# Optimization experiments

Hardware: AMD Instinct MI355X
Metric: run time of the kernel (lower is better)

The kernel has to match this reference:

```python
import jax, jax.numpy as jnp
import numpy as np

B, N, NFEAT = 8, 5000, 15
NUM_CLASSES_IN = 12          # len(elem_labels)
D_IN = NUM_CLASSES_IN + NFEAT - 1  # 26
D_DIST = 256
D_HID = 256
BIN_SIZE = 100
NBINS = N // BIN_SIZE        # 50
K = 16                       # num_neighbors
DIST_MULT = 0.1
MAX_HALF_BINS = 100          # max_num_bins // 2
NUM_ID_OUT, NUM_REG_OUT = 8, 4


def _pairwise_dist(A):
    # A: [nbins, bs, d] -> [nbins, bs, bs]
    na = jnp.sum(A * A, -1)
    d2 = na[..., :, None] - 2.0 * jnp.einsum('...nd,...md->...nm', A, A) + na[..., None, :]
    return jnp.sqrt(jnp.maximum(d2, 1e-6))


def _build_edges(points, rot):
    # points: [N, D_DIST]; LSH binning then per-bin kNN (exp(-dist_mult * dist) affinities)
    mul = points @ rot[:, :NBINS // 2]
    cmul = jnp.concatenate([mul, -mul], axis=-1)
    bin_idx = jnp.argmax(cmul, axis=-1)
    bins_split = jnp.argsort(bin_idx).reshape(NBINS, BIN_SIZE)   # [nbins, bs] point ids
    parts = points[bins_split]                                   # [nbins, bs, d]
    dm = jnp.exp(-DIST_MULT * _pairwise_dist(parts))             # [nbins, bs, bs]
    vals, idx = jax.lax.top_k(dm, K)                             # [nbins, bs, K]
    dst = jax.vmap(lambda b, i: b[i])(bins_split, idx)           # global dst ids
    src = jnp.broadcast_to(bins_split[:, :, None], dst.shape)
    return src.reshape(-1), dst.reshape(-1), vals.reshape(-1)    # nnz = N*K


def _ghconv(x, src, dst, vals, theta, W_h, W_t, b_t):
    # x: [N, H]; edge list (src, dst, vals); duplicates sum, matching tf.sparse.add
    deg = jax.ops.segment_sum(vals, src, num_segments=N)
    norm = jnp.power(deg + 1e-6, -0.5)[:, None]
    f_hom = (x @ theta) * norm
    agg = jax.ops.segment_sum(vals[:, None] * f_hom[dst], src, num_segments=N) * norm
    f_het = x @ W_h
    gate = jax.nn.sigmoid(x @ W_t + b_t)
    return jax.nn.selu(gate * agg + (1.0 - gate) * f_het)


def setup_inputs() -> dict:
    key = jax.random.key(0)
    ks = jax.random.split(key, 32)
    w = lambda i, shape, s=0.02: (s * jax.random.normal(ks[i], shape)).astype(jnp.float32)
    ids = jax.random.randint(ks[0], (B, N, 1), 0, NUM_CLASSES_IN).astype(jnp.float32)
    props = jax.random.normal(ks[1], (B, N, NFEAT - 1), dtype=jnp.float32)
    X = jnp.concatenate([ids, props], axis=-1)
    return {
        'X': X,
        'rot': w(2, (D_DIST, MAX_HALF_BINS), 1.0),
        'W_emb': w(3, (D_IN, D_DIST)), 'b_emb': w(4, (D_DIST,)),
        'Wenc_id': w(5, (D_IN, D_HID)), 'benc_id': w(6, (D_HID,)),
        'theta_id': w(7, (D_HID, D_HID)), 'Wh_id': w(8, (D_HID, D_HID)),
        'Wt_id': w(9, (D_HID, D_HID)), 'bt_id': w(10, (D_HID,)),
        'Wdec_id': w(11, (D_HID, D_HID)), 'bdec_id': w(12, (D_HID,)),
        'Wout_id': w(13, (D_HID, NUM_ID_OUT)), 'bout_id': w(14, (NUM_ID_OUT,)),
        'Wenc_reg': w(15, (D_IN, D_HID)), 'benc_reg': w(16, (D_HID,)),
        'theta_reg': w(17, (D_HID, D_HID)), 'Wh_reg': w(18, (D_HID, D_HID)),
        'Wt_reg': w(19, (D_HID, D_HID)), 'bt_reg': w(20, (D_HID,)),
        'Wdec_reg': w(21, (D_HID, D_HID)), 'bdec_reg': w(22, (D_HID,)),
        'Wout_reg': w(23, (D_HID, NUM_REG_OUT)), 'bout_reg': w(24, (NUM_REG_OUT,)),
    }


def reference(X, rot, W_emb, b_emb,
              Wenc_id, benc_id, theta_id, Wh_id, Wt_id, bt_id, Wdec_id, bdec_id, Wout_id, bout_id,
              Wenc_reg, benc_reg, theta_reg, Wh_reg, Wt_reg, bt_reg, Wdec_reg, bdec_reg, Wout_reg, bout_reg):
    # InputEncoding: one-hot class id + remaining features
    enc = jnp.concatenate(
        [jax.nn.one_hot(X[:, :, 0].astype(jnp.int32), NUM_CLASSES_IN, dtype=jnp.float32),
         X[:, :, 1:]], axis=-1)                                  # [B, N, 26]
    emb = enc @ W_emb + b_emb                                     # distance embedding
    src, dst, vals = jax.vmap(_build_edges, in_axes=(0, None))(emb, rot)

    def branch(Wenc, benc, theta, Wh, Wt, bt, Wdec, bdec, Wout, bout):
        x = jax.nn.selu(enc @ Wenc + benc)
        x = jax.vmap(lambda xb, s, d, v: _ghconv(xb, s, d, v, theta, Wh, Wt, bt))(x, src, dst, vals)
        x = jax.nn.selu(x @ Wdec + bdec)
        return x @ Wout + bout

    out_id = branch(Wenc_id, benc_id, theta_id, Wh_id, Wt_id, bt_id, Wdec_id, bdec_id, Wout_id, bout_id)
    out_reg = branch(Wenc_reg, benc_reg, theta_reg, Wh_reg, Wt_reg, bt_reg, Wdec_reg, bdec_reg, Wout_reg, bout_reg)
    return out_id, out_reg
```

## Files before the change

kernel.cpp:

```cpp
#include <hip/hip_runtime.h>
#include <hip/hip_bf16.h>
#include <cstdint>
#include <cstddef>

#define NB     8
#define NLOC   5000
#define NPTS   40000
#define DIN    26
#define DH     256
#define NBINS  50
#define BSZ    100
#define KNN    16
#define KP     104

static const size_t OFF_BHI0  = 40960000;
static const size_t OFF_BLO0  = 41353216;
static const size_t OFF_BDHI0 = 41746432;
static const size_t OFF_BDLO0 = 41877504;
static const size_t OFF_BHI1  = 42100000;
static const size_t OFF_BLO1  = 42493216;
static const size_t OFF_BDHI1 = 42886432;
static const size_t OFF_BDLO1 = 43017504;
static const size_t OFF_ENC   = 81920000;
static const size_t OFF_BIN   = 86080000;
static const size_t OFF_ORD   = 86240000;
static const size_t OFF_NRM   = 86400000;
static const size_t OFF_EVAL  = 86560000;
static const size_t OFF_EDST  = 89120000;
static const size_t OFF_KEYS  = 91680000;
static const size_t OFF_AXHI  = 91680000;
static const size_t OFF_AXLO  = 112160000;
static const size_t OFF_NA    = 132640000;
static const size_t OFF_FHET  = 132640000;
static const size_t OFF_GATE  = 173600000;

typedef __attribute__((ext_vector_type(8))) short short8;
typedef __attribute__((ext_vector_type(4))) float f32x4;

__device__ __forceinline__ float selu_f(float x) {
  const float scale = 1.0507009873554805f, alpha = 1.6732632423543772f;
  return x > 0.f ? scale * x : scale * alpha * expm1f(x);
}

__device__ __forceinline__ void split_bf16(float v, __hip_bfloat16& h, __hip_bfloat16& l) {
  h = __float2bfloat16(v);
  l = __float2bfloat16(v - __bfloat162float(h));
}

#define EPB 16
__global__ __launch_bounds__(256) void k_enc_emb(
    const float* __restrict__ X, const float* __restrict__ Wemb,
    const float* __restrict__ bemb, float* __restrict__ enc,
    double* __restrict__ emb, double* __restrict__ na_u) {
  __shared__ float xb[EPB * 15];
  __shared__ double partd[EPB][4];
  const int tid = threadIdx.x;
  const int lane = tid & 63, wid = tid >> 6;
  const int r0 = blockIdx.x * EPB;
  if (tid < EPB * 15) xb[tid] = X[(size_t)r0 * 15 + tid];
  double wcol[DIN];
  #pragma unroll
  for (int c = 0; c < DIN; c++) wcol[c] = (double)Wemb[c * DH + tid];
  const double bcol = (double)bemb[tid];
  __syncthreads();
  #pragma unroll 1
  for (int p = 0; p < EPB; p++) {
    const int id = (int)xb[p * 15];
    double acc = 0.0;
    #pragma unroll
    for (int c = 0; c < 12; c++)
      acc += ((c == id) ? 1.0 : 0.0) * wcol[c];
    #pragma unroll
    for (int c = 12; c < DIN; c++)
      acc += (double)xb[p * 15 + (c - 11)] * wcol[c];
    const double v = acc + bcol;
    emb[(size_t)(r0 + p) * DH + tid] = v;
    double sq = v * v;
    #pragma unroll
    for (int off = 32; off >= 1; off >>= 1) sq += __shfl_xor(sq, off);
    if (lane == 0) partd[p][wid] = sq;
  }
  __syncthreads();
  if (tid < EPB)
    na_u[r0 + tid] = partd[tid][0] + partd[tid][1] + partd[tid][2] + partd[tid][3];
  #pragma unroll
  for (int t = 0; t < 2; t++) {
    int idx = t * 256 + tid;
    if (idx < EPB * DIN) {
      int p = idx / DIN, c = idx - p * DIN;
      int id = (int)xb[p * 15];
      float v = (c < 12) ? ((c == id) ? 1.f : 0.f) : xb[p * 15 + (c - 11)];
      enc[(size_t)(r0 + p) * DIN + c] = v;
    }
  }
}

#define MULPTS 16
__global__ __launch_bounds__(512) void k_mul(
    const double* __restrict__ emb, const float* __restrict__ rot,
    int* __restrict__ bin_idx) {
  __shared__ double ebuf[MULPTS][258];
  __shared__ float  rotT[25][257];
  __shared__ double mulb[MULPTS][26];
  const int tid = threadIdx.x;
  const int r0 = blockIdx.x * MULPTS;
  for (int idx = tid; idx < 25 * DH; idx += 512) {
    int d = idx / 25, j = idx - d * 25;
    rotT[j][d] = rot[d * 100 + j];
  }
  for (int idx = tid; idx < MULPTS * DH; idx += 512) {
    int p = idx >> 8, d = idx & 255;
    ebuf[p][d] = emb[(size_t)(r0 + p) * DH + d];
  }
  __syncthreads();
  if (tid < MULPTS * 25) {
    int p = tid / 25, j = tid - p * 25;
    double a = 0.0;
    #pragma unroll 4
    for (int d = 0; d < DH; d++) a += ebuf[p][d] * (double)rotT[j][d];
    mulb[p][j] = a;
  }
  __syncthreads();
  if (tid < MULPTS) {
    double best = -1e300; int bi = 0;
    #pragma unroll 1
    for (int jj = 0; jj < 2 * 25; jj++) {
      double v = (jj < 25) ? mulb[tid][jj] : -mulb[tid][jj - 25];
      if (v > best) { best = v; bi = jj; }
    }
    bin_idx[r0 + tid] = bi;
  }
}

#define SCH 20
__global__ __launch_bounds__(256) void k_sort(
    const int* __restrict__ bin_idx, int* __restrict__ order) {
  const int b = blockIdx.x;
  __shared__ unsigned short cnt[256][NBINS + 2];
  __shared__ int base[NBINS];
  __shared__ int bl[NLOC];
  const int tid = threadIdx.x;
  for (int j = 0; j < NBINS; j++) cnt[tid][j] = 0;
  for (int n = tid; n < NLOC; n += 256) bl[n] = bin_idx[b * NLOC + n];
  __syncthreads();
  const int s = tid * SCH;
  const int e = (s + SCH < NLOC) ? s + SCH : NLOC;
  for (int n = s; n < e; n++) cnt[tid][bl[n]]++;
  __syncthreads();
  if (tid < NBINS) {
    int run = 0;
    for (int t = 0; t < 256; t++) {
      int c = cnt[t][tid];
      cnt[t][tid] = (unsigned short)run;
      run += c;
    }
    base[tid] = run;
  }
  __syncthreads();
  if (tid == 0) {
    int r = 0;
    for (int j = 0; j < NBINS; j++) { int t = base[j]; base[j] = r; r += t; }
  }
  __syncthreads();
  for (int n = s; n < e; n++) {
    int j = bl[n];
    int pos = base[j] + cnt[tid][j];
    cnt[tid][j]++;
    order[b * NLOC + pos] = n;
  }
}

#define DQR 112
__global__ __launch_bounds__(256) void k_dist(
    const double* __restrict__ emb, const int* __restrict__ order,
    const double* __restrict__ na_u, double* __restrict__ keys) {
  __shared__ double P[DQR][34];
  __shared__ double naL[DQR];
  __shared__ int rid[DQR];
  const int bin = blockIdx.x;
  const int gb0 = bin * BSZ;
  const int brow = (bin / NBINS) * NLOC;
  const int tid = threadIdx.x;
  const int tx = tid & 15, ty = tid >> 4;
  if (tid < DQR) {
    int rr = tid < BSZ ? tid : BSZ - 1;
    int g = brow + order[gb0 + rr];
    rid[tid] = g;
    naL[tid] = na_u[g];
  }
  __syncthreads();
  size_t srow[7];
  int scol[7], sr[7];
  #pragma unroll
  for (int q = 0; q < 7; q++) {
    int idx = q * 256 + tid;
    sr[q] = idx >> 4;
    scol[q] = (idx & 15) * 2;
    srow[q] = (size_t)rid[sr[q]] * DH;
  }
  double acc[7][7] = {};
  double2 buf[7];
  #pragma unroll
  for (int q = 0; q < 7; q++)
    buf[q] = *(const double2*)&emb[srow[q] + scol[q]];
  for (int kc = 0; kc < 8; kc++) {
    __syncthreads();
    #pragma unroll
    for (int q = 0; q < 7; q++) {
      P[sr[q]][scol[q]]     = buf[q].x;
      P[sr[q]][scol[q] + 1] = buf[q].y;
    }
    __syncthreads();
    if (kc < 7) {
      #pragma unroll
      for (int q = 0; q < 7; q++)
        buf[q] = *(const double2*)&emb[srow[q] + (kc + 1) * 32 + scol[q]];
    }
    #pragma unroll 1
    for (int kk = 0; kk < 32; kk += 2) {
      double2 b2[7], a2[7];
      #pragma unroll
      for (int j = 0; j < 7; j++) b2[j] = *(const double2*)&P[tx + 16 * j][kk];
      #pragma unroll
      for (int i = 0; i < 7; i++) a2[i] = *(const double2*)&P[ty + 16 * i][kk];
      #pragma unroll
      for (int i = 0; i < 7; i++)
        #pragma unroll
        for (int j = 0; j < 7; j++) acc[i][j] += a2[i].x * b2[j].x;
      #pragma unroll
      for (int i = 0; i < 7; i++)
        #pragma unroll
        for (int j = 0; j < 7; j++) acc[i][j] += a2[i].y * b2[j].y;
    }
  }
  #pragma unroll
  for (int i = 0; i < 7; i++) {
    int gi = ty + 16 * i;
    if (gi >= BSZ) continue;
    #pragma unroll
    for (int j = 0; j < 7; j++) {
      int gj = tx + 16 * j;
      if (gj >= BSZ) continue;
      double t = naL[gi] - 2.0 * acc[i][j];
      t += naL[gj];
      keys[(size_t)(gb0 + gi) * KP + gj] = (t > 1e-6) ? t : 1e-6;
    }
  }
}

__global__ __launch_bounds__(256) void k_topk(
    const double* __restrict__ keys, float* __restrict__ evals,
    int* __restrict__ edstl, float* __restrict__ normv) {
  const int g = threadIdx.x >> 4;
  const int l = threadIdx.x & 15;
  const int row = blockIdx.x * 16 + g;
  const unsigned long long* kr =
      (const unsigned long long*)(keys + (size_t)row * KP);
  unsigned long long c[7];
  #pragma unroll
  for (int s = 0; s < 7; s++) {
    int j = s * 16 + l;
    c[s] = (j < BSZ) ? kr[j] : ~0ull;
  }
  float deg = 0.f, myev = 0.f;
  int myidx = 0;
  #pragma unroll 1
  for (int k = 0; k < KNN; k++) {
    unsigned long long mv = c[0];
    int ms = 0;
    #pragma unroll
    for (int s = 1; s < 7; s++)
      if (c[s] < mv) { mv = c[s]; ms = s; }
    int idx = ms * 16 + l;
    #pragma unroll
    for (int off = 8; off >= 1; off >>= 1) {
      unsigned long long ov = __shfl_xor(mv, off);
      int oi = __shfl_xor(idx, off);
      if (ov < mv || (ov == mv && oi < idx)) { mv = ov; idx = oi; }
    }
    float ev = expf(-0.1f * sqrtf((float)__longlong_as_double(mv)));
    deg += ev;
    if (l == k) { myev = ev; myidx = idx; }
    const int own = idx & 15, slot = idx >> 4;
    if (l == own) {
      #pragma unroll
      for (int s = 0; s < 7; s++)
        if (slot == s) c[s] = ~0ull;
    }
  }
  evals[(size_t)row * KNN + l] = myev;
  edstl[(size_t)row * KNN + l] = myidx;
  if (l == 0) normv[row] = 1.f / sqrtf(deg + 1e-6f);
}

#define XPB 16
__global__ __launch_bounds__(256) void k_encmm(
    const float* __restrict__ enc, const float* __restrict__ W,
    const float* __restrict__ bias, __hip_bfloat16* __restrict__ hi,
    __hip_bfloat16* __restrict__ lo) {
  __shared__ float eb[XPB * DIN];
  const int tid = threadIdx.x;
  const int r0 = blockIdx.x * XPB;
  for (int idx = tid; idx < XPB * DIN; idx += 256)
    eb[idx] = enc[(size_t)r0 * DIN + idx];
  float wcol[DIN];
  #pragma unroll
  for (int c = 0; c < DIN; c++) wcol[c] = W[c * DH + tid];
  const float bcol = bias[tid];
  __syncthreads();
  #pragma unroll 1
  for (int p = 0; p < XPB; p++) {
    float acc = 0.f;
    #pragma unroll
    for (int c = 0; c < DIN; c++) acc += eb[p * DIN + c] * wcol[c];
    float v = selu_f(acc + bcol);
    __hip_bfloat16 h, l;
    split_bf16(v, h, l);
    hi[(size_t)(r0 + p) * DH + tid] = h;
    lo[(size_t)(r0 + p) * DH + tid] = l;
  }
}

__global__ __launch_bounds__(256) void k_cvt_w8(
    const float* __restrict__ W0, const float* __restrict__ W1,
    const float* __restrict__ W2, const float* __restrict__ W3,
    const float* __restrict__ W4, const float* __restrict__ W5,
    const float* __restrict__ W6, const float* __restrict__ W7,
    __hip_bfloat16* __restrict__ Bhi0, __hip_bfloat16* __restrict__ Blo0,
    __hip_bfloat16* __restrict__ Bdhi0, __hip_bfloat16* __restrict__ Bdlo0,
    __hip_bfloat16* __restrict__ Bhi1, __hip_bfloat16* __restrict__ Blo1,
    __hip_bfloat16* __restrict__ Bdhi1, __hip_bfloat16* __restrict__ Bdlo1) {
  __shared__ float t[32][33];
  const int z = blockIdx.z;
  const float* W = (z == 0) ? W0 : (z == 1) ? W1 : (z == 2) ? W2 : (z == 3) ? W3
                 : (z == 4) ? W4 : (z == 5) ? W5 : (z == 6) ? W6 : W7;
  const int zz = z & 3, br = z >> 2;
  __hip_bfloat16* hi = (zz < 3) ? (br ? Bhi1 : Bhi0) + (size_t)zz * 65536
                                : (br ? Bdhi1 : Bdhi0);
  __hip_bfloat16* lo = (zz < 3) ? (br ? Blo1 : Blo0) + (size_t)zz * 65536
                                : (br ? Bdlo1 : Bdlo0);
  const int tid = threadIdx.x, tx = tid & 31, ty = tid >> 5;
  const int k0 = blockIdx.x * 32, n0 = blockIdx.y * 32;
  #pragma unroll
  for (int r = 0; r < 4; r++)
    t[ty + r * 8][tx] = W[(size_t)(k0 + ty + r * 8) * 256 + n0 + tx];
  __syncthreads();
  #pragma unroll
  for (int r = 0; r < 4; r++) {
    int n = ty + r * 8;
    float v = t[tx][n];
    __hip_bfloat16 h, l;
    split_bf16(v, h, l);
    hi[(size_t)(n0 + n) * 256 + k0 + tx] = h;
    lo[(size_t)(n0 + n) * 256 + k0 + tx] = l;
  }
}

#define MF_SMEM (4 * 128 * 40 * 2)
template <int MODE>
__global__ __launch_bounds__(256, 4) void k_mfma(
    const ushort* __restrict__ Ahi, const ushort* __restrict__ Alo,
    const ushort* __restrict__ Bhi, const ushort* __restrict__ Blo,
    const float* __restrict__ bias,
    float* __restrict__ O0, float* __restrict__ O1, float* __restrict__ O2) {
  extern __shared__ char mfs[];
  short* As0 = (short*)mfs;
  short* As1 = As0 + 128 * 40;
  short* Bs0 = As1 + 128 * 40;
  short* Bs1 = Bs0 + 128 * 40;
  const int NX = (MODE == 0) ? 6 : 2;
  const int total = NX * 313;
  const int q = total >> 3, rr8 = total & 7;
  const int xcd = blockIdx.x & 7, pos = blockIdx.x >> 3;
  const int lw = (xcd < rr8 ? xcd * (q + 1) : rr8 * (q + 1) + (xcd - rr8) * q) + pos;
  const int m0 = (lw / NX) * 128;
  const int nx = lw - (lw / NX) * NX;
  const int n0 = nx * 128;
  const int tid = threadIdx.x;
  const int lane = tid & 63, wid = tid >> 6;
  const int wr = wid >> 1, wc = wid & 1;
  const int lm = lane & 15, lg = lane >> 4;
  f32x4 acc[4][4];
  #pragma unroll
  for (int i = 0; i < 4; i++)
    #pragma unroll
    for (int j = 0; j < 4; j++)
      #pragma unroll
      for (int r = 0; r < 4; r++) acc[i][j][r] = 0.f;

  for (int k0 = 0; k0 < 256; k0 += 32) {
    #pragma unroll
    for (int it = 0; it < 2; it++) {
      int idx = it * 256 + tid;
      int r = idx >> 2, c = (idx & 3) * 8;
      int gm = m0 + r; if (gm >= NPTS) gm = NPTS - 1;
      *(uint4*)&As0[r * 40 + c] = *(const uint4*)&Ahi[(size_t)gm * 256 + k0 + c];
      *(uint4*)&As1[r * 40 + c] = *(const uint4*)&Alo[(size_t)gm * 256 + k0 + c];
      *(uint4*)&Bs0[r * 40 + c] = *(const uint4*)&Bhi[(size_t)(n0 + r) * 256 + k0 + c];
      *(uint4*)&Bs1[r * 40 + c] = *(const uint4*)&Blo[(size_t)(n0 + r) * 256 + k0 + c];
    }
    __syncthreads();
    const int lk = lg * 8;
    short8 aH[4], bH[4], aL[4], bL[4];
    #pragma unroll
    for (int mf = 0; mf < 4; mf++)
      aH[mf] = *(const short8*)&As0[(wr * 64 + mf * 16 + lm) * 40 + lk];
    #pragma unroll
    for (int nf = 0; nf < 4; nf++)
      bH[nf] = *(const short8*)&Bs0[(wc * 64 + nf * 16 + lm) * 40 + lk];
    #pragma unroll
    for (int mf = 0; mf < 4; mf++)
      #pragma unroll
      for (int nf = 0; nf < 4; nf++)
        acc[mf][nf] = __builtin_amdgcn_mfma_f32_16x16x32_bf16(aH[mf], bH[nf], acc[mf][nf], 0, 0, 0);
    #pragma unroll
    for (int nf = 0; nf < 4; nf++)
      bL[nf] = *(const short8*)&Bs1[(wc * 64 + nf * 16 + lm) * 40 + lk];
    #pragma unroll
    for (int mf = 0; mf < 4; mf++)
      #pragma unroll
      for (int nf = 0; nf < 4; nf++)
        acc[mf][nf] = __builtin_amdgcn_mfma_f32_16x16x32_bf16(aH[mf], bL[nf], acc[mf][nf], 0, 0, 0);
    #pragma unroll
    for (int mf = 0; mf < 4; mf++)
      aL[mf] = *(const short8*)&As1[(wr * 64 + mf * 16 + lm) * 40 + lk];
    #pragma unroll
    for (int mf = 0; mf < 4; mf++)
      #pragma unroll
      for (int nf = 0; nf < 4; nf++)
        acc[mf][nf] = __builtin_amdgcn_mfma_f32_16x16x32_bf16(aL[mf], bH[nf], acc[mf][nf], 0, 0, 0);
    __syncthreads();
  }

  float* Out; int cb;
  if (MODE == 0) {
    const int seg = nx >> 1;
    Out = (seg == 0) ? O0 : ((seg == 1) ? O1 : O2);
    cb = (nx & 1) * 128;
  } else {
    Out = O0; cb = n0;
  }
  const bool do_gate = (MODE == 0) && (nx >> 1) == 2;
  #pragma unroll
  for (int mf = 0; mf < 4; mf++) {
    const int gm0 = m0 + wr * 64 + mf * 16 + lg * 4;
    #pragma unroll
    for (int nf = 0; nf < 4; nf++) {
      const int gn = cb + wc * 64 + nf * 16 + lm;
      #pragma unroll
      for (int r = 0; r < 4; r++) {
        const int gm = gm0 + r;
        if (gm >= NPTS) continue;
        float c = acc[mf][nf][r];
        if (MODE == 1)      c = selu_f(c + bias[gn]);
        else if (do_gate)   c = 1.f / (1.f + expf(-(c + bias[gn])));
        Out[(size_t)gm * 256 + gn] = c;
      }
    }
  }
}

#define GAT_SMEM (100 * 256 * 4 + 1600 * 8 + 100 * 4 + 100 * 4)
__global__ __launch_bounds__(1024) void k_gatherb(
    const float* __restrict__ hth, const float* __restrict__ fhet,
    const float* __restrict__ gate, const float* __restrict__ evals,
    const int* __restrict__ edstl, const int* __restrict__ order,
    const float* __restrict__ normv, __hip_bfloat16* __restrict__ yhi,
    __hip_bfloat16* __restrict__ ylo) {
  extern __shared__ char gsm[];
  float*  hl  = (float*)gsm;
  float2* cwL = (float2*)(gsm + 102400);
  int*    idsL = (int*)(gsm + 102400 + 12800);
  float*  nvL  = (float*)(gsm + 102400 + 12800 + 400);
  const int bin = blockIdx.x;
  const int gb0 = bin * 100;
  const int brow = (bin / NBINS) * NLOC;
  const int tid = threadIdx.x;
  const int p = tid >> 8, d = tid & 255;
  if (tid < BSZ) {
    idsL[tid] = order[gb0 + tid];
    nvL[tid] = normv[gb0 + tid];
  }
  __syncthreads();
  for (int t = tid; t < BSZ * KNN; t += 1024) {
    int lj = edstl[(size_t)gb0 * KNN + t];
    cwL[t] = make_float2(evals[(size_t)gb0 * KNN + t] * nvL[lj],
                         __int_as_float(lj));
  }
  for (int idx = tid; idx < BSZ * DH; idx += 1024) {
    int i = idx >> 8, dd = idx & 255;
    hl[i * 256 + dd] = hth[(size_t)(brow + idsL[i]) * DH + dd];
  }
  __syncthreads();
  size_t srow_n = (size_t)(brow + idsL[p]) * DH;
  float g_n = gate[srow_n + d], fh_n = fhet[srow_n + d];
  #pragma unroll 1
  for (int ii = 0; ii < 25; ii++) {
    const int i = ii * 4 + p;
    const size_t srow = srow_n;
    const float g = g_n, fh = fh_n;
    if (ii < 24) {
      srow_n = (size_t)(brow + idsL[i + 4]) * DH;
      g_n = gate[srow_n + d];
      fh_n = fhet[srow_n + d];
    }
    float acc = 0.f;
    #pragma unroll
    for (int k = 0; k < KNN; k++) {
      float2 cw = cwL[i * KNN + k];
      acc += cw.x * hl[__float_as_int(cw.y) * 256 + d];
    }
    float v = selu_f(g * (nvL[i] * acc) + (1.f - g) * fh);
    __hip_bfloat16 h, l;
    split_bf16(v, h, l);
    yhi[srow + d] = h;
    ylo[srow + d] = l;
  }
}

template <int OW>
__global__ __launch_bounds__(256) void k_out(
    const float* __restrict__ Z, const float* __restrict__ W,
    const float* __restrict__ bias, float* __restrict__ out) {
  const int p0 = blockIdx.x * 32;
  __shared__ float zb[32][257];
  const int tid = threadIdx.x;
  for (int idx = tid; idx < 32 * DH; idx += 256) {
    int p = idx >> 8, d = idx & 255;
    zb[p][d] = Z[(size_t)(p0 + p) * DH + d];
  }
  __syncthreads();
  if (tid < 32 * OW) {
    int p = tid / OW, o = tid - (tid / OW) * OW;
    float acc = 0.f;
    #pragma unroll 4
    for (int d = 0; d < DH; d++) acc += zb[p][d] * W[d * OW + o];
    out[(size_t)(p0 + p) * OW + o] = acc + bias[o];
  }
}

extern "C" void kernel_launch(void* const* d_in, const int* in_sizes, int n_in,
                              void* d_out, int out_size, void* d_ws, size_t ws_size,
                              hipStream_t stream) {
  const float* X     = (const float*)d_in[0];
  const float* rot   = (const float*)d_in[1];
  const float* W_emb = (const float*)d_in[2];
  const float* b_emb = (const float*)d_in[3];
  const float* Wenc[2]  = {(const float*)d_in[4],  (const float*)d_in[14]};
  const float* benc[2]  = {(const float*)d_in[5],  (const float*)d_in[15]};
  const float* theta[2] = {(const float*)d_in[6],  (const float*)d_in[16]};
  const float* Wh[2]    = {(const float*)d_in[7],  (const float*)d_in[17]};
  const float* Wt[2]    = {(const float*)d_in[8],  (const float*)d_in[18]};
  const float* bt[2]    = {(const float*)d_in[9],  (const float*)d_in[19]};
  const float* Wdec[2]  = {(const float*)d_in[10], (const float*)d_in[20]};
  const float* bdec[2]  = {(const float*)d_in[11], (const float*)d_in[21]};
  const float* Wout[2]  = {(const float*)d_in[12], (const float*)d_in[22]};
  const float* bout[2]  = {(const float*)d_in[13], (const float*)d_in[23]};

  char* w = (char*)d_ws;
  double* emb   = (double*)(w + 0);
  float*  hth   = (float*)(w + 0);
  __hip_bfloat16* Bhi[2]  = {(__hip_bfloat16*)(w + OFF_BHI0),  (__hip_bfloat16*)(w + OFF_BHI1)};
  __hip_bfloat16* Blo[2]  = {(__hip_bfloat16*)(w + OFF_BLO0),  (__hip_bfloat16*)(w + OFF_BLO1)};
  __hip_bfloat16* Bdhi[2] = {(__hip_bfloat16*)(w + OFF_BDHI0), (__hip_bfloat16*)(w + OFF_BDHI1)};
  __hip_bfloat16* Bdlo[2] = {(__hip_bfloat16*)(w + OFF_BDLO0), (__hip_bfloat16*)(w + OFF_BDLO1)};
  float*  enc   = (float*)(w + OFF_ENC);
  int*    binid = (int*)(w + OFF_BIN);
  int*    order = (int*)(w + OFF_ORD);
  float*  normv = (float*)(w + OFF_NRM);
  float*  evals = (float*)(w + OFF_EVAL);
  int*    edstl = (int*)(w + OFF_EDST);
  double* keys  = (double*)(w + OFF_KEYS);
  double* na_u  = (double*)(w + OFF_NA);
  __hip_bfloat16* Axhi = (__hip_bfloat16*)(w + OFF_AXHI);
  __hip_bfloat16* Axlo = (__hip_bfloat16*)(w + OFF_AXLO);
  float*  fhet  = (float*)(w + OFF_FHET);
  float*  gate  = (float*)(w + OFF_GATE);
  float*  zbuf  = (float*)(w + OFF_GATE);
  float*  outp  = (float*)d_out;

  (void)hipFuncSetAttribute(reinterpret_cast<const void*>(k_gatherb),
                            hipFuncAttributeMaxDynamicSharedMemorySize, GAT_SMEM);
  (void)hipFuncSetAttribute(reinterpret_cast<const void*>(k_mfma<0>),
                            hipFuncAttributeMaxDynamicSharedMemorySize, MF_SMEM);
  (void)hipFuncSetAttribute(reinterpret_cast<const void*>(k_mfma<1>),
                            hipFuncAttributeMaxDynamicSharedMemorySize, MF_SMEM);

  k_enc_emb<<<NPTS / EPB, 256, 0, stream>>>(X, W_emb, b_emb, enc, emb, na_u);
  k_mul<<<NPTS / MULPTS, 512, 0, stream>>>(emb, rot, binid);
  k_sort<<<NB, 256, 0, stream>>>(binid, order);
  k_dist<<<NB * NBINS, 256, 0, stream>>>(emb, order, na_u, keys);
  k_topk<<<NPTS / 16, 256, 0, stream>>>(keys, evals, edstl, normv);
  k_cvt_w8<<<dim3(8, 8, 8), 256, 0, stream>>>(
      theta[0], Wh[0], Wt[0], Wdec[0], theta[1], Wh[1], Wt[1], Wdec[1],
      Bhi[0], Blo[0], Bdhi[0], Bdlo[0], Bhi[1], Blo[1], Bdhi[1], Bdlo[1]);

  for (int br = 0; br < 2; br++) {
    k_encmm<<<NPTS / XPB, 256, 0, stream>>>(enc, Wenc[br], benc[br], Axhi, Axlo);
    k_mfma<0><<<6 * 313, 256, MF_SMEM, stream>>>((const ushort*)Axhi, (const ushort*)Axlo,
                                                 (const ushort*)Bhi[br], (const ushort*)Blo[br],
                                                 bt[br], hth, fhet, gate);
    k_gatherb<<<NB * NBINS, 1024, GAT_SMEM, stream>>>(hth, fhet, gate, evals, edstl,
                                                      order, normv, Axhi, Axlo);
    k_mfma<1><<<2 * 313, 256, MF_SMEM, stream>>>((const ushort*)Axhi, (const ushort*)Axlo,
                                                 (const ushort*)Bdhi[br], (const ushort*)Bdlo[br],
                                                 bdec[br], zbuf, nullptr, nullptr);
    if (br == 0) k_out<8><<<NPTS / 32, 256, 0, stream>>>(zbuf, Wout[0], bout[0], outp);
    else         k_out<4><<<NPTS / 32, 256, 0, stream>>>(zbuf, Wout[1], bout[1], outp + (size_t)NPTS * 8);
  }
}
```

Baseline: 658.4 us.

## Stage MFMA GEMM tiles via direct global-to-LDS loads with XOR swizzle and K=64

Replaces register-staged uint4 copies into padded LDS with global_load_lds DMA-style loads into an XOR-swizzled 64-wide LDS layout. The K step doubles from 32 to 64, halving the number of barrier-separated load phases, and the launch-bounds occupancy hint is dropped. This aims to cut VGPR traffic and LDS bank conflicts during staging. The trade-off is twice the shared memory per block (64 KB), which may lower occupancy, and there is still no double buffering.

Result: slower. 686.6 us (+4.3%).

```diff
diff --git a/kernel.cpp b/kernel.cpp
--- a/kernel.cpp
+++ b/kernel.cpp
@@ -47,6 +47,12 @@
   l = __float2bfloat16(v - __bfloat162float(h));
 }
 
+__device__ __forceinline__ void gl16(const void* g, void* l) {
+  __builtin_amdgcn_global_load_lds(
+      (const __attribute__((address_space(1))) void*)g,
+      (__attribute__((address_space(3))) void*)l, 16, 0, 0);
+}
+
 #define EPB 16
 __global__ __launch_bounds__(256) void k_enc_emb(
     const float* __restrict__ X, const float* __restrict__ Wemb,
@@ -356,18 +362,18 @@
   }
 }
 
-#define MF_SMEM (4 * 128 * 40 * 2)
+#define MF_SMEM (4 * 128 * 64 * 2)
 template <int MODE>
-__global__ __launch_bounds__(256, 4) void k_mfma(
+__global__ __launch_bounds__(256) void k_mfma(
     const ushort* __restrict__ Ahi, const ushort* __restrict__ Alo,
     const ushort* __restrict__ Bhi, const ushort* __restrict__ Blo,
     const float* __restrict__ bias,
     float* __restrict__ O0, float* __restrict__ O1, float* __restrict__ O2) {
   extern __shared__ char mfs[];
   short* As0 = (short*)mfs;
-  short* As1 = As0 + 128 * 40;
-  short* Bs0 = As1 + 128 * 40;
-  short* Bs1 = Bs0 + 128 * 40;
+  short* As1 = As0 + 128 * 64;
+  short* Bs0 = As1 + 128 * 64;
+  short* Bs1 = Bs0 + 128 * 64;
   const int NX = (MODE == 0) ? 6 : 2;
   const int total = NX * 313;
   const int q = total >> 3, rr8 = total & 7;
@@ -380,6 +386,8 @@
   const int lane = tid & 63, wid = tid >> 6;
   const int wr = wid >> 1, wc = wid & 1;
   const int lm = lane & 15, lg = lane >> 4;
+  const int lrow = lane >> 3;
+  const int csw8 = ((lane & 7) ^ lrow) << 3;
   f32x4 acc[4][4];
   #pragma unroll
   for (int i = 0; i < 4; i++)
@@ -388,48 +396,69 @@
       #pragma unroll
       for (int r = 0; r < 4; r++) acc[i][j][r] = 0.f;
 
-  for (int k0 = 0; k0 < 256; k0 += 32) {
-    #pragma unroll
-    for (int it = 0; it < 2; it++) {
-      int idx = it * 256 + tid;
-      int r = idx >> 2, c = (idx & 3) * 8;
-      int gm = m0 + r; if (gm >= NPTS) gm = NPTS - 1;
-      *(uint4*)&As0[r * 40 + c] = *(const uint4*)&Ahi[(size_t)gm * 256 + k0 + c];
-      *(uint4*)&As1[r * 40 + c] = *(const uint4*)&Alo[(size_t)gm * 256 + k0 + c];
-      *(uint4*)&Bs0[r * 40 + c] = *(const uint4*)&Bhi[(size_t)(n0 + r) * 256 + k0 + c];
-      *(uint4*)&Bs1[r * 40 + c] = *(const uint4*)&Blo[(size_t)(n0 + r) * 256 + k0 + c];
-    }
-    __syncthreads();
-    const int lk = lg * 8;
-    short8 aH[4], bH[4], aL[4], bL[4];
-    #pragma unroll
-    for (int mf = 0; mf < 4; mf++)
-      aH[mf] = *(const short8*)&As0[(wr * 64 + mf * 16 + lm) * 40 + lk];
-    #pragma unroll
-    for (int nf = 0; nf < 4; nf++)
-      bH[nf] = *(const short8*)&Bs0[(wc * 64 + nf * 16 + lm) * 40 + lk];
-    #pragma unroll
-    for (int mf = 0; mf < 4; mf++)
-      #pragma unroll
-      for (int nf = 0; nf < 4; nf++)
-        acc[mf][nf] = __builtin_amdgcn_mfma_f32_16x16x32_bf16(aH[mf], bH[nf], acc[mf][nf], 0, 0, 0);
-    #pragma unroll
-    for (int nf = 0; nf < 4; nf++)
-      bL[nf] = *(const short8*)&Bs1[(wc * 64 + nf * 16 + lm) * 40 + lk];
-    #pragma unroll
-    for (int mf = 0; mf < 4; mf++)
-      #pragma unroll
-      for (int nf = 0; nf < 4; nf++)
-        acc[mf][nf] = __builtin_amdgcn_mfma_f32_16x16x32_bf16(aH[mf], bL[nf], acc[mf][nf], 0, 0, 0);
-    #pragma unroll
-    for (int mf = 0; mf < 4; mf++)
-      aL[mf] = *(const short8*)&As1[(wr * 64 + mf * 16 + lm) * 40 + lk];
-    #pragma unroll
-    for (int mf = 0; mf < 4; mf++)
-      #pragma unroll
-      for (int nf = 0; nf < 4; nf++)
-        acc[mf][nf] = __builtin_amdgcn_mfma_f32_16x16x32_bf16(aL[mf], bH[nf], acc[mf][nf], 0, 0, 0);
-    __syncthreads();
+  auto STAGE = [&](int k0) {
+    #pragma unroll
+    for (int t = 0; t < 4; t++) {
+      const int rl = wid * 32 + t * 8;
+      const int r = rl + lrow;
+      int gmA = m0 + r; if (gmA >= NPTS) gmA = NPTS - 1;
+      const size_t ga = (size_t)gmA * 256 + k0 + csw8;
+      const size_t gb = (size_t)(n0 + r) * 256 + k0 + csw8;
+      gl16(Ahi + ga, As0 + rl * 64);
+      gl16(Alo + ga, As1 + rl * 64);
+      gl16(Bhi + gb, Bs0 + rl * 64);
+      gl16(Blo + gb, Bs1 + rl * 64);
+    }
+  };
+
+  STAGE(0);
+  __syncthreads();
+  for (int ks = 0; ks < 4; ks++) {
+    #pragma unroll
+    for (int kk = 0; kk < 2; kk++) {
+      const int ch = kk * 4 + lg;
+      short8 aH[4], bH[4], aL[4], bL[4];
+      #pragma unroll
+      for (int mf = 0; mf < 4; mf++) {
+        const int row = wr * 64 + mf * 16 + lm;
+        aH[mf] = *(const short8*)&As0[row * 64 + ((ch ^ (lm & 7)) << 3)];
+      }
+      #pragma unroll
+      for (int nf = 0; nf < 4; nf++) {
+        const int row = wc * 64 + nf * 16 + lm;
+        bH[nf] = *(const short8*)&Bs0[row * 64 + ((ch ^ (lm & 7)) << 3)];
+      }
+      #pragma unroll
+      for (int mf = 0; mf < 4; mf++)
+        #pragma unroll
+        for (int nf = 0; nf < 4; nf++)
+          acc[mf][nf] = __builtin_amdgcn_mfma_f32_16x16x32_bf16(aH[mf], bH[nf], acc[mf][nf], 0, 0, 0);
+      #pragma unroll
+      for (int nf = 0; nf < 4; nf++) {
+        const int row = wc * 64 + nf * 16 + lm;
+        bL[nf] = *(const short8*)&Bs1[row * 64 + ((ch ^ (lm & 7)) << 3)];
+      }
+      #pragma unroll
+      for (int mf = 0; mf < 4; mf++)
+        #pragma unroll
+        for (int nf = 0; nf < 4; nf++)
+          acc[mf][nf] = __builtin_amdgcn_mfma_f32_16x16x32_bf16(aH[mf], bL[nf], acc[mf][nf], 0, 0, 0);
+      #pragma unroll
+      for (int mf = 0; mf < 4; mf++) {
+        const int row = wr * 64 + mf * 16 + lm;
+        aL[mf] = *(const short8*)&As1[row * 64 + ((ch ^ (lm & 7)) << 3)];
+      }
+      #pragma unroll
+      for (int mf = 0; mf < 4; mf++)
+        #pragma unroll
+        for (int nf = 0; nf < 4; nf++)
+          acc[mf][nf] = __builtin_amdgcn_mfma_f32_16x16x32_bf16(aL[mf], bH[nf], acc[mf][nf], 0, 0, 0);
+    }
+    if (ks < 3) {
+      __syncthreads();
+      STAGE((ks + 1) * 64);
+      __syncthreads();
+    }
   }
 
   float* Out; int cb;
```
